# Performance work log

Hardware: AMD Instinct MI355X
Metric: run time of the kernel (lower is better)

The kernel has to match this reference:

```python
import jax, jax.numpy as jnp
import numpy as np

B, N, T, F, D, R, K, L, E = 4, 2000, 50, 10, 64, 8, 16, 3, 32


def setup_inputs() -> dict:
    key = jax.random.key(0)
    ks = jax.random.split(key, 12)
    rn = lambda k, shape, sc: (jax.random.normal(k, shape, jnp.float32) * sc)
    return {
        "X": jax.random.normal(ks[0], (B, N, T, F), jnp.float32),
        "neighbors": jax.random.randint(ks[1], (B, R, N, K), 0, N + 1),
        "gru_W": rn(ks[2], (F, 3 * D), 0.1),
        "gru_U": rn(ks[3], (D, 3 * D), 0.1),
        "gru_b": jnp.zeros((2, 3 * D), jnp.float32),
        "rel_emb": rn(ks[4], (R, E), 0.1),
        "proj_W": rn(ks[5], (R, D, D), 0.05),
        "proj_b": jnp.zeros((R, D), jnp.float32),
        "satt_W": rn(ks[6], (R, 2 * D + E), 0.05),
        "satt_b": jnp.zeros((R,), jnp.float32),
        "ratt_W": rn(ks[7], (2 * D + E,), 0.05),
        "ratt_b": jnp.zeros((), jnp.float32),
        "pred_W": rn(ks[8], (D, L), 0.05),
        "pred_b": jnp.zeros((L,), jnp.float32),
    }


def leaky(x):  # tf.nn.leaky_relu default alpha=0.2
    return jnp.where(x >= 0, x, 0.2 * x)


def gru(x, W, U, b):
    # Keras GRU (reset_after=True), gate order [z, r, h]. x: (M, T, F)
    xp = x @ W + b[0]                      # (M, T, 3D) input projections, precomputed
    h0 = jnp.zeros((x.shape[0], U.shape[0]), x.dtype)

    def step(h, xt):
        rec = h @ U + b[1]
        xz, xr, xh = jnp.split(xt, 3, axis=-1)
        rz, rr, rh = jnp.split(rec, 3, axis=-1)
        z = jax.nn.sigmoid(xz + rz)
        r = jax.nn.sigmoid(xr + rr)
        hh = jnp.tanh(xh + r * rh)
        return z * h + (1.0 - z) * hh, None

    h, _ = jax.lax.scan(step, h0, jnp.swapaxes(xp, 0, 1))
    return h


def reference(X, neighbors, gru_W, gru_U, gru_b, rel_emb, proj_W, proj_b,
              satt_W, satt_b, ratt_W, ratt_b, pred_W, pred_b):
    b, n, t, f = X.shape
    d = gru_U.shape[0]

    # --- GRU feature extraction (dropout inactive at inference) ---
    node = gru(X.reshape(b * n, t, f), gru_W, gru_U, gru_b).reshape(b, n, d)
    padded = jnp.concatenate([jnp.zeros((b, 1, d), node.dtype), node], axis=1)  # (B, N+1, D)

    # --- per-relation neighbor gather + projection ---
    neigh_raw = jax.vmap(lambda nf, idx: nf[idx])(padded, neighbors)            # (B, R, N, K, D)
    neigh = leaky(jnp.einsum('brnkd,rde->brnke', neigh_raw, proj_W)
                  + proj_b[None, :, None, None, :])                              # (B, R, N, K, D)

    cur = node                                                                   # (B, N, D)

    # --- state attention: Dense(1) on concat[cur, neigh, rel_emb], split weights ---
    w_cur, w_ngh, w_rel = satt_W[:, :d], satt_W[:, d:2 * d], satt_W[:, 2 * d:]
    s_cur = jnp.einsum('bnd,rd->brn', cur, w_cur)                                # (B, R, N)
    s_ngh = jnp.einsum('brnkd,rd->brnk', neigh, w_ngh)                           # (B, R, N, K)
    s_rel = jnp.einsum('re,re->r', rel_emb, w_rel) + satt_b                      # (R,)
    scores = leaky(s_cur[:, :, :, None] + s_ngh + s_rel[None, :, None, None])
    scores = scores + jnp.where(neighbors == 0, -1e9, 0.0).astype(scores.dtype)  # mask padding node
    att = jax.nn.softmax(scores, axis=-1)                                        # over K
    rel_rep = jnp.einsum('brnk,brnkd->brnd', att, neigh)                         # (B, R, N, D)

    # --- relation attention ---
    rep_t = jnp.transpose(rel_rep, (0, 2, 1, 3))                                 # (B, N, R, D)
    r_cur, r_rep, r_emb = ratt_W[:d], ratt_W[d:2 * d], ratt_W[2 * d:]
    rs = leaky(jnp.einsum('bnd,d->bn', cur, r_cur)[:, :, None]
               + jnp.einsum('bnrd,d->bnr', rep_t, r_rep)
               + (rel_emb @ r_emb)[None, None, :] + ratt_b)                      # (B, N, R)
    ratt = jax.nn.softmax(rs, axis=-1)
    agg = jnp.einsum('bnr,bnrd->bnd', ratt, rep_t)
    updated = cur + agg

    # --- prediction head ---
    return jax.nn.softmax(updated @ pred_W + pred_b)
```

## Files before the change

### kernel.cpp

```cpp
#include <hip/hip_runtime.h>
#include <hip/hip_bf16.h>
#include <cstddef>

constexpr int cB=4, cN=2000, cT=50, cF=10, cD=64, cR=8, cK=16, cE=32;
constexpr int NODES = cB*cN;
constexpr int N1    = cN+1;
constexpr int ROWS2 = cB*N1;

#define DEV static __device__ __forceinline__

typedef __attribute__((ext_vector_type(8))) short bf16x8;
typedef __attribute__((ext_vector_type(4))) float f32x4;
typedef __attribute__((ext_vector_type(4))) int   i32x4;

DEV float leaky(float x){ return fmaxf(x, 0.2f*x); }
DEV float wsumall(float v){
  v += __shfl_xor(v,32,64); v += __shfl_xor(v,16,64); v += __shfl_xor(v,8,64);
  v += __shfl_xor(v,4,64);  v += __shfl_xor(v,2,64);  v += __shfl_xor(v,1,64);
  return v;
}
DEV unsigned fu(float f){ return __float_as_uint(f); }
DEV float hif(float f){ return __uint_as_float(fu(f) & 0xFFFF0000u); }
DEV unsigned rne16(float f){
  unsigned u = fu(f);
  return (u + 0x7FFFu + ((u>>16)&1u)) >> 16;
}
DEV bf16x8 pack4(unsigned a, unsigned b, unsigned c2, unsigned d){
  union { i32x4 i; bf16x8 h; } u;
  u.i = (i32x4){(int)a,(int)b,(int)c2,(int)d};
  return u.h;
}
DEV unsigned PLO(unsigned x, unsigned y){ return __builtin_amdgcn_perm(y, x, 0x05040100u); }
DEV unsigned PHI(unsigned x, unsigned y){ return __builtin_amdgcn_perm(y, x, 0x07060302u); }
DEV f32x4 MF(bf16x8 a, bf16x8 b, f32x4 c){
  return __builtin_amdgcn_mfma_f32_16x16x32_bf16(a, b, c, 0, 0, 0);
}
DEV float bfu(unsigned short u){ return __uint_as_float(((unsigned)u)<<16); }

__global__ __launch_bounds__(256, 2) void k_gru(const float* __restrict__ X,
    const float* __restrict__ gW, const float* __restrict__ gU,
    const float* __restrict__ gb, const float* __restrict__ pW,
    const float* __restrict__ pb, const float* __restrict__ sattW,
    float* __restrict__ node, unsigned short* __restrict__ actb,
    float* __restrict__ sng2)
{
  __shared__ unsigned sH[2][1024];

  const int tid  = threadIdx.x;
  const int lane = tid & 63;
  const int w    = tid >> 6;
  const int c    = lane & 15;
  const int kg   = lane >> 4;
  const int nb   = (int)blockIdx.x * 16;
  const int col  = 16*w + c;
  const int bb   = nb / cN;

  bf16x8 BUhi[2][3], BUlo[2][3], BX[3];
  #pragma unroll
  for (int s=0;s<2;++s){
    #pragma unroll
    for (int cls=0; cls<3; ++cls){
      const int n = cls*64 + col;
      unsigned hi[4], lo[4];
      #pragma unroll
      for (int p=0;p<4;++p){
        float u0 = gU[(s*32 + kg*8 + 2*p    )*192 + n];
        float u1 = gU[(s*32 + kg*8 + 2*p + 1)*192 + n];
        hi[p] = (fu(u0)>>16) | (fu(u1) & 0xFFFF0000u);
        lo[p] = rne16(u0 - hif(u0)) | (rne16(u1 - hif(u1)) << 16);
      }
      BUhi[s][cls] = pack4(hi[0],hi[1],hi[2],hi[3]);
      BUlo[s][cls] = pack4(lo[0],lo[1],lo[2],lo[3]);
    }
  }
  #pragma unroll
  for (int cls=0; cls<3; ++cls){
    const int n = cls*64 + col;
    unsigned wd[4];
    #pragma unroll
    for (int p=0;p<4;++p){
      int f = kg*4 + p;
      unsigned v = (f < cF) ? rne16(gW[f*192 + n]) : 0u;
      wd[p] = v | (v << 16);
    }
    BX[cls] = pack4(wd[0],wd[1],wd[2],wd[3]);
  }

  const float bz  = gb[col]      + gb[192+col];
  const float br  = gb[64+col]   + gb[256+col];
  const float bh0 = gb[128+col];
  const float bh1 = gb[320+col];

  for (int i2 = tid; i2 < 1024; i2 += 256) sH[0][i2] = 0u;
  f32x4 ho = {0.f,0.f,0.f,0.f};
  __syncthreads();

  float xc[4], xn[4];
  const float* Xb = X + (size_t)(nb + c)*cT*cF;
  {
    #pragma unroll
    for (int p=0;p<4;++p){ int f = 4*kg+p; xc[p] = (f < cF) ? Xb[0*cF + f] : 0.f; }
    #pragma unroll
    for (int p=0;p<4;++p){ int f = 4*kg+p; xn[p] = (f < cF) ? Xb[1*cF + f] : 0.f; }
  }

  const unsigned sw  = (unsigned)((c&7)<<2);
  const unsigned rb0 = (unsigned)(c*64 + kg*8);

  for (int t = 0; t < cT; ++t){
    unsigned xw[4];
    #pragma unroll
    for (int p=0;p<4;++p)
      xw[p] = (fu(xc[p])>>16) | (rne16(xc[p] - hif(xc[p])) << 16);
    bf16x8 xf = pack4(xw[0],xw[1],xw[2],xw[3]);

    #pragma unroll
    for (int p=0;p<4;++p) xc[p] = xn[p];
    {
      int tn = (t+2 < cT) ? t+2 : cT-1;
      #pragma unroll
      for (int p=0;p<4;++p){ int f = 4*kg+p; xn[p] = (f < cF) ? Xb[(size_t)tn*cF + f] : 0.f; }
    }

    const unsigned* sr = sH[t & 1];
    i32x4 qa = *(const i32x4*)(sr + ((rb0 +  0) ^ sw));
    i32x4 qb = *(const i32x4*)(sr + ((rb0 +  4) ^ sw));
    i32x4 qc = *(const i32x4*)(sr + ((rb0 + 32) ^ sw));
    i32x4 qd = *(const i32x4*)(sr + ((rb0 + 36) ^ sw));
    bf16x8 hh0 = pack4(PLO(qa[0],qa[1]), PLO(qa[2],qa[3]), PLO(qb[0],qb[1]), PLO(qb[2],qb[3]));
    bf16x8 hl0 = pack4(PHI(qa[0],qa[1]), PHI(qa[2],qa[3]), PHI(qb[0],qb[1]), PHI(qb[2],qb[3]));
    bf16x8 hh1 = pack4(PLO(qc[0],qc[1]), PLO(qc[2],qc[3]), PLO(qd[0],qd[1]), PLO(qd[2],qd[3]));
    bf16x8 hl1 = pack4(PHI(qc[0],qc[1]), PHI(qc[2],qc[3]), PHI(qd[0],qd[1]), PHI(qd[2],qd[3]));

    f32x4 aZ  = {bz,bz,bz,bz};
    f32x4 aR  = {br,br,br,br};
    f32x4 aHc = {bh1,bh1,bh1,bh1};
    f32x4 aXh = {bh0,bh0,bh0,bh0};
    aZ  = MF(xf, BX[0], aZ);
    aR  = MF(xf, BX[1], aR);
    aXh = MF(xf, BX[2], aXh);
    aZ  = MF(hh0, BUhi[0][0], aZ);  aZ  = MF(hh1, BUhi[1][0], aZ);
    aR  = MF(hh0, BUhi[0][1], aR);  aR  = MF(hh1, BUhi[1][1], aR);
    aHc = MF(hh0, BUhi[0][2], aHc); aHc = MF(hh1, BUhi[1][2], aHc);
    aZ  = MF(hl0, BUhi[0][0], aZ);  aZ  = MF(hl1, BUhi[1][0], aZ);
    aR  = MF(hl0, BUhi[0][1], aR);  aR  = MF(hl1, BUhi[1][1], aR);
    aHc = MF(hl0, BUhi[0][2], aHc); aHc = MF(hl1, BUhi[1][2], aHc);
    aZ  = MF(hh0, BUlo[0][0], aZ);  aZ  = MF(hh1, BUlo[1][0], aZ);
    aR  = MF(hh0, BUlo[0][1], aR);  aR  = MF(hh1, BUlo[1][1], aR);
    aHc = MF(hh0, BUlo[0][2], aHc); aHc = MF(hh1, BUlo[1][2], aHc);

    unsigned* swr = sH[(t & 1) ^ 1];
    #pragma unroll
    for (int reg=0; reg<4; ++reg){
      float z  = __builtin_amdgcn_rcpf(1.0f + __expf(-aZ[reg]));
      float r  = __builtin_amdgcn_rcpf(1.0f + __expf(-aR[reg]));
      float pre = __builtin_fmaf(r, aHc[reg], aXh[reg]);
      float th = 1.0f - 2.0f*__builtin_amdgcn_rcpf(__expf(2.0f*pre) + 1.0f);
      float hn = __builtin_fmaf(z, ho[reg]-th, th);
      ho[reg] = hn;
      unsigned val = (fu(hn)>>16) | (rne16(hn - hif(hn)) << 16);
      int nodei = kg*4 + reg;
      swr[((unsigned)(nodei*64 + col)) ^ ((unsigned)((nodei&7)<<2))] = val;
    }
    asm volatile("s_waitcnt lgkmcnt(0)" ::: "memory");
    __builtin_amdgcn_s_barrier();
  }

  #pragma unroll
  for (int reg=0; reg<4; ++reg)
    node[(size_t)(nb + kg*4 + reg)*cD + col] = ho[reg];

  {
    const unsigned* sr = &sH[0][0];
    i32x4 qa = *(const i32x4*)(sr + ((rb0 +  0) ^ sw));
    i32x4 qb = *(const i32x4*)(sr + ((rb0 +  4) ^ sw));
    i32x4 qc = *(const i32x4*)(sr + ((rb0 + 32) ^ sw));
    i32x4 qd = *(const i32x4*)(sr + ((rb0 + 36) ^ sw));
    bf16x8 hh0 = pack4(PLO(qa[0],qa[1]), PLO(qa[2],qa[3]), PLO(qb[0],qb[1]), PLO(qb[2],qb[3]));
    bf16x8 hl0 = pack4(PHI(qa[0],qa[1]), PHI(qa[2],qa[3]), PHI(qb[0],qb[1]), PHI(qb[2],qb[3]));
    bf16x8 hh1 = pack4(PLO(qc[0],qc[1]), PLO(qc[2],qc[3]), PLO(qd[0],qd[1]), PLO(qd[2],qd[3]));
    bf16x8 hl1 = pack4(PHI(qc[0],qc[1]), PHI(qc[2],qc[3]), PHI(qd[0],qd[1]), PHI(qd[2],qd[3]));

    const int qbase = nb + bb + 1;
    #pragma unroll
    for (int r2=0; r2<2; ++r2){
      const int r = 2*w + r2;
      const float* Pr = pW + (size_t)r*cD*cD;
      bf16x8 PB[4][2];
      float pbv[4], wnv[4];
      #pragma unroll
      for (int cb=0; cb<4; ++cb){
        const int e = 16*cb + c;
        #pragma unroll
        for (int s=0;s<2;++s){
          unsigned wd[4];
          #pragma unroll
          for (int p=0;p<4;++p){
            int k0 = s*32 + kg*8 + 2*p;
            wd[p] = rne16(Pr[(size_t)k0*cD + e]) | (rne16(Pr[(size_t)(k0+1)*cD + e]) << 16);
          }
          PB[cb][s] = pack4(wd[0],wd[1],wd[2],wd[3]);
        }
        pbv[cb] = pb[r*cD + e];
        wnv[cb] = sattW[r*(2*cD+cE) + cD + e];
      }
      float sp[4] = {0.f,0.f,0.f,0.f};
      #pragma unroll
      for (int cb=0; cb<4; ++cb){
        f32x4 acc = {pbv[cb],pbv[cb],pbv[cb],pbv[cb]};
        acc = MF(hh0, PB[cb][0], acc); acc = MF(hh1, PB[cb][1], acc);
        acc = MF(hl0, PB[cb][0], acc); acc = MF(hl1, PB[cb][1], acc);
        #pragma unroll
        for (int reg=0; reg<4; ++reg){
          float o = leaky(acc[reg]);
          int qrow = qbase + kg*4 + reg;
          actb[((size_t)r*ROWS2 + qrow)*cD + 16*cb + c] = (unsigned short)rne16(o);
          sp[reg] = __builtin_fmaf(o, wnv[cb], sp[reg]);
        }
      }
      #pragma unroll
      for (int reg=0; reg<4; ++reg){
        float s2 = sp[reg];
        s2 += __shfl_xor(s2,1,64); s2 += __shfl_xor(s2,2,64);
        s2 += __shfl_xor(s2,4,64); s2 += __shfl_xor(s2,8,64);
        if (c == 0) sng2[(size_t)r*ROWS2 + qbase + kg*4 + reg] = s2;
      }
    }
  }

  if ((blockIdx.x % (cN/16)) == 0){
    #pragma unroll
    for (int r2=0; r2<2; ++r2){
      const int r = 2*w + r2;
      float v0 = leaky(pb[r*cD + lane]);
      float wv = sattW[r*(2*cD+cE) + cD + lane];
      actb[((size_t)r*ROWS2 + (size_t)bb*N1)*cD + lane] = (unsigned short)rne16(v0);
      float s2 = wsumall(v0 * wv);
      if (lane == 0) sng2[(size_t)r*ROWS2 + (size_t)bb*N1] = s2;
    }
  }
}

__global__ __launch_bounds__(256) void k_attn(const float* __restrict__ node,
    const int* __restrict__ nbrs, const float* __restrict__ sattW,
    const float* __restrict__ sattb, const float* __restrict__ rattW,
    const float* __restrict__ rattb, const float* __restrict__ predW,
    const float* __restrict__ predb, const float* __restrict__ relemb,
    const unsigned short* __restrict__ actb, const float* __restrict__ sng2,
    float* __restrict__ out)
{
  __shared__ float sSA[cR][cD];
  __shared__ float sSrel[cR], sRremb[cR];
  __shared__ float sAtt[4][cR][cK];
  __shared__ int   sOff[4][cR][cK];
  const int tid = threadIdx.x;
  for (int i=tid; i<cR*cD; i+=256) sSA[i>>6][i&63] = sattW[(i>>6)*(2*cD+cE) + (i&63)];
  if (tid < 64){
    int r = tid >> 3, j0 = (tid & 7)*4;
    float a = 0.f, b2 = 0.f;
    #pragma unroll
    for (int j=0;j<4;++j){
      float re = relemb[r*cE + j0 + j];
      a  += re * sattW[r*(2*cD+cE) + 2*cD + j0 + j];
      b2 += re * rattW[2*cD + j0 + j];
    }
    a  += __shfl_xor(a,1,64);  a  += __shfl_xor(a,2,64);  a  += __shfl_xor(a,4,64);
    b2 += __shfl_xor(b2,1,64); b2 += __shfl_xor(b2,2,64); b2 += __shfl_xor(b2,4,64);
    if ((tid & 7) == 0){ sSrel[r] = a + sattb[r]; sRremb[r] = b2; }
  }
  __syncthreads();

  const int wave = tid >> 6, lane = tid & 63;
  const int gn = (int)blockIdx.x*4 + wave;
  const int b = __builtin_amdgcn_readfirstlane(gn / cN);
  const int n = __builtin_amdgcn_readfirstlane(gn % cN);

  const float cur = node[(size_t)gn*cD + lane];

  float scr[8];
  #pragma unroll
  for (int r=0; r<8; ++r) scr[r] = wsumall(cur * sSA[r][lane]);

  const int g = lane >> 4, k = lane & 15;
  #pragma unroll
  for (int half=0; half<2; ++half){
    int r = half*4 + g;
    float sc0 = half==0 ? (g==0?scr[0]:g==1?scr[1]:g==2?scr[2]:scr[3])
                        : (g==0?scr[4]:g==1?scr[5]:g==2?scr[6]:scr[7]);
    int idx = nbrs[(((size_t)b*cR + r)*cN + n)*cK + k];
    int o = r*ROWS2 + b*N1 + idx;
    float sv = sng2[o];
    float sc = leaky(sc0 + sv + sSrel[r]);
// ... 30 lines not shown
  float rs[8];
  #pragma unroll
  for (int r=0; r<8; ++r) rs[r] = leaky(c0 + wsumall(facc[r]*rrep) + sRremb[r] + rb);
  float mx = rs[0];
  #pragma unroll
  for (int r=1; r<8; ++r) mx = fmaxf(mx, rs[r]);
  float es = 0.f; float ratt[8];
  #pragma unroll
  for (int r=0; r<8; ++r){ ratt[r] = __expf(rs[r]-mx); es += ratt[r]; }
  float inv = 1.f/es;
  float agg = 0.f;
  #pragma unroll
  for (int r=0; r<8; ++r) agg += (ratt[r]*inv) * facc[r];
  const float upd = cur + agg;

  float l0 = wsumall(upd * predW[lane*3 + 0]);
  float l1 = wsumall(upd * predW[lane*3 + 1]);
  float l2 = wsumall(upd * predW[lane*3 + 2]);
  if (lane == 0){
    l0 += predb[0]; l1 += predb[1]; l2 += predb[2];
    float m2 = fmaxf(l0, fmaxf(l1, l2));
    float e0 = __expf(l0-m2), e1 = __expf(l1-m2), e2 = __expf(l2-m2);
    float is = 1.f/(e0+e1+e2);
    out[(size_t)gn*3+0] = e0*is;
    out[(size_t)gn*3+1] = e1*is;
    out[(size_t)gn*3+2] = e2*is;
  }
}

extern "C" void kernel_launch(void* const* d_in, const int* in_sizes, int n_in,
                              void* d_out, int out_size, void* d_ws, size_t ws_size,
                              hipStream_t stream)
{
  const float* X      = (const float*)d_in[0];
  const int*   nbrs   = (const int*)  d_in[1];
  const float* gW     = (const float*)d_in[2];
  const float* gU     = (const float*)d_in[3];
  const float* gb     = (const float*)d_in[4];
  const float* relemb = (const float*)d_in[5];
  const float* pW     = (const float*)d_in[6];
  const float* pb     = (const float*)d_in[7];
  const float* sattW  = (const float*)d_in[8];
  const float* sattb  = (const float*)d_in[9];
  const float* rattW  = (const float*)d_in[10];
  const float* rattb  = (const float*)d_in[11];
  const float* predW  = (const float*)d_in[12];
  const float* predb  = (const float*)d_in[13];
  float* out = (float*)d_out;

  float*          node  = (float*)d_ws;
  unsigned short* actb  = (unsigned short*)(node + (size_t)NODES*cD);
  float*          sng2  = (float*)(actb + (size_t)cR*ROWS2*cD);

  k_gru <<<NODES/16, 256, 0, stream>>>(X, gW, gU, gb, pW, pb, sattW,
                                       node, actb, sng2);
  k_attn<<<NODES/4, 256, 0, stream>>>(node, nbrs, sattW, sattb, rattW, rattb,
                                      predW, predb, relemb, actb, sng2, out);
}
```

Baseline: 88.80 us.

## Split GRU recurrent K-dimension across two wave groups with LDS partial-sum exchange

```diff
diff --git a/kernel.cpp b/kernel.cpp
--- a/kernel.cpp
+++ b/kernel.cpp
@@ -32,12 +32,17 @@
 }
 DEV unsigned PLO(unsigned x, unsigned y){ return __builtin_amdgcn_perm(y, x, 0x05040100u); }
 DEV unsigned PHI(unsigned x, unsigned y){ return __builtin_amdgcn_perm(y, x, 0x07060302u); }
+DEV unsigned pack_hl3(float f){
+  float rem = f - hif(f);
+  return PHI(fu(f), fu(rem));
+}
 DEV f32x4 MF(bf16x8 a, bf16x8 b, f32x4 c){
   return __builtin_amdgcn_mfma_f32_16x16x32_bf16(a, b, c, 0, 0, 0);
 }
 DEV float bfu(unsigned short u){ return __uint_as_float(((unsigned)u)<<16); }
-
-__global__ __launch_bounds__(256, 2) void k_gru(const float* __restrict__ X,
+DEV float ex2(float x){ float r; asm("v_exp_f32 %0, %1" : "=v"(r) : "v"(x)); return r; }
+
+__global__ __launch_bounds__(512, 4) void k_gru(const float* __restrict__ X,
     const float* __restrict__ gW, const float* __restrict__ gU,
     const float* __restrict__ gb, const float* __restrict__ pW,
     const float* __restrict__ pb, const float* __restrict__ sattW,
@@ -45,53 +50,60 @@
     float* __restrict__ sng2)
 {
   __shared__ unsigned sH[2][1024];
+  __shared__ __align__(16) float pP[4][3][256];
 
   const int tid  = threadIdx.x;
   const int lane = tid & 63;
-  const int w    = tid >> 6;
+  const int w8   = tid >> 6;
+  const int w    = w8 & 3;
+  const bool owner = (w8 < 4);
+  const int s    = owner ? 0 : 1;
   const int c    = lane & 15;
   const int kg   = lane >> 4;
   const int nb   = (int)blockIdx.x * 16;
   const int col  = 16*w + c;
   const int bb   = nb / cN;
 
-  bf16x8 BUhi[2][3], BUlo[2][3], BX[3];
-  #pragma unroll
-  for (int s=0;s<2;++s){
-    #pragma unroll
-    for (int cls=0; cls<3; ++cls){
-      const int n = cls*64 + col;
-      unsigned hi[4], lo[4];
-      #pragma unroll
-      for (int p=0;p<4;++p){
-        float u0 = gU[(s*32 + kg*8 + 2*p    )*192 + n];
-        float u1 = gU[(s*32 + kg*8 + 2*p + 1)*192 + n];
-        hi[p] = (fu(u0)>>16) | (fu(u1) & 0xFFFF0000u);
-        lo[p] = rne16(u0 - hif(u0)) | (rne16(u1 - hif(u1)) << 16);
-      }
-      BUhi[s][cls] = pack4(hi[0],hi[1],hi[2],hi[3]);
-      BUlo[s][cls] = pack4(lo[0],lo[1],lo[2],lo[3]);
-    }
-  }
+  const float SZ = -1.4426950408889634f;
+  const float SH =  2.8853900817779268f;
+
+  const float scl0 = SZ, scl1 = SZ, scl2 = SH;
+  bf16x8 Uhi[3], Ulo[3], BXv[3];
   #pragma unroll
   for (int cls=0; cls<3; ++cls){
+    const float sc = (cls==2) ? scl2 : (cls==1 ? scl1 : scl0);
+    const int n = cls*64 + col;
+    unsigned hi[4], lo[4];
+    #pragma unroll
+    for (int p=0;p<4;++p){
+      float u0 = sc * gU[(s*32 + kg*8 + 2*p    )*192 + n];
+      float u1 = sc * gU[(s*32 + kg*8 + 2*p + 1)*192 + n];
+      hi[p] = (fu(u0)>>16) | (fu(u1) & 0xFFFF0000u);
+      lo[p] = rne16(u0 - hif(u0)) | (rne16(u1 - hif(u1)) << 16);
+    }
+    Uhi[cls] = pack4(hi[0],hi[1],hi[2],hi[3]);
+    Ulo[cls] = pack4(lo[0],lo[1],lo[2],lo[3]);
+  }
+  #pragma unroll
+  for (int cls=0; cls<3; ++cls){
+    const float sc = (cls==2) ? scl2 : scl0;
     const int n = cls*64 + col;
     unsigned wd[4];
     #pragma unroll
     for (int p=0;p<4;++p){
       int f = kg*4 + p;
-      unsigned v = (f < cF) ? rne16(gW[f*192 + n]) : 0u;
+      unsigned v = (f < cF) ? rne16(sc * gW[f*192 + n]) : 0u;
       wd[p] = v | (v << 16);
     }
-    BX[cls] = pack4(wd[0],wd[1],wd[2],wd[3]);
-  }
-
-  const float bz  = gb[col]      + gb[192+col];
-  const float br  = gb[64+col]   + gb[256+col];
-  const float bh0 = gb[128+col];
-  const float bh1 = gb[320+col];
-
-  for (int i2 = tid; i2 < 1024; i2 += 256) sH[0][i2] = 0u;
+    BXv[cls] = pack4(wd[0],wd[1],wd[2],wd[3]);
+  }
+
+  const float bz  = SZ*(gb[col]      + gb[192+col]);
+  const float br  = SZ*(gb[64+col]   + gb[256+col]);
+  const float bh0 = SH* gb[128+col];
+  const float bh1 = SH* gb[320+col];
+
+  for (int i2 = tid; i2 < 1024; i2 += 512) sH[0][i2] = 0u;
   f32x4 ho = {0.f,0.f,0.f,0.f};
   __syncthreads();
 
@@ -106,69 +118,94 @@
 
   const unsigned sw  = (unsigned)((c&7)<<2);
   const unsigned rb0 = (unsigned)(c*64 + kg*8);
+  float* pw0 = &pP[w][0][c*16 + kg*4];
+  float* pw1 = &pP[w][1][c*16 + kg*4];
+  float* pw2 = &pP[w][2][c*16 + kg*4];
 
   for (int t = 0; t < cT; ++t){
-    unsigned xw[4];
-    #pragma unroll
-    for (int p=0;p<4;++p)
-      xw[p] = (fu(xc[p])>>16) | (rne16(xc[p] - hif(xc[p])) << 16);
-    bf16x8 xf = pack4(xw[0],xw[1],xw[2],xw[3]);
-
-    #pragma unroll
-    for (int p=0;p<4;++p) xc[p] = xn[p];
-    {
-      int tn = (t+2 < cT) ? t+2 : cT-1;
+    const unsigned* sr = sH[t & 1];
+    f32x4 aZ, aR, aHc, aXh;
+    if (owner){
+      bf16x8 xf = pack4(pack_hl3(xc[0]), pack_hl3(xc[1]),
+                        pack_hl3(xc[2]), pack_hl3(xc[3]));
       #pragma unroll
-      for (int p=0;p<4;++p){ int f = 4*kg+p; xn[p] = (f < cF) ? Xb[(size_t)tn*cF + f] : 0.f; }
-    }
-
-    const unsigned* sr = sH[t & 1];
-    i32x4 qa = *(const i32x4*)(sr + ((rb0 +  0) ^ sw));
-    i32x4 qb = *(const i32x4*)(sr + ((rb0 +  4) ^ sw));
-    i32x4 qc = *(const i32x4*)(sr + ((rb0 + 32) ^ sw));
-    i32x4 qd = *(const i32x4*)(sr + ((rb0 + 36) ^ sw));
-    bf16x8 hh0 = pack4(PLO(qa[0],qa[1]), PLO(qa[2],qa[3]), PLO(qb[0],qb[1]), PLO(qb[2],qb[3]));
-    bf16x8 hl0 = pack4(PHI(qa[0],qa[1]), PHI(qa[2],qa[3]), PHI(qb[0],qb[1]), PHI(qb[2],qb[3]));
-    bf16x8 hh1 = pack4(PLO(qc[0],qc[1]), PLO(qc[2],qc[3]), PLO(qd[0],qd[1]), PLO(qd[2],qd[3]));
-    bf16x8 hl1 = pack4(PHI(qc[0],qc[1]), PHI(qc[2],qc[3]), PHI(qd[0],qd[1]), PHI(qd[2],qd[3]));
-
-    f32x4 aZ  = {bz,bz,bz,bz};
-    f32x4 aR  = {br,br,br,br};
-    f32x4 aHc = {bh1,bh1,bh1,bh1};
-    f32x4 aXh = {bh0,bh0,bh0,bh0};
-    aZ  = MF(xf, BX[0], aZ);
-    aR  = MF(xf, BX[1], aR);
-    aXh = MF(xf, BX[2], aXh);
-    aZ  = MF(hh0, BUhi[0][0], aZ);  aZ  = MF(hh1, BUhi[1][0], aZ);
-    aR  = MF(hh0, BUhi[0][1], aR);  aR  = MF(hh1, BUhi[1][1], aR);
-    aHc = MF(hh0, BUhi[0][2], aHc); aHc = MF(hh1, BUhi[1][2], aHc);
-    aZ  = MF(hl0, BUhi[0][0], aZ);  aZ  = MF(hl1, BUhi[1][0], aZ);
-    aR  = MF(hl0, BUhi[0][1], aR);  aR  = MF(hl1, BUhi[1][1], aR);
-    aHc = MF(hl0, BUhi[0][2], aHc); aHc = MF(hl1, BUhi[1][2], aHc);
-    aZ  = MF(hh0, BUlo[0][0], aZ);  aZ  = MF(hh1, BUlo[1][0], aZ);
-    aR  = MF(hh0, BUlo[0][1], aR);  aR  = MF(hh1, BUlo[1][1], aR);
-    aHc = MF(hh0, BUlo[0][2], aHc); aHc = MF(hh1, BUlo[1][2], aHc);
-
-    unsigned* swr = sH[(t & 1) ^ 1];
-    #pragma unroll
-    for (int reg=0; reg<4; ++reg){
-      float z  = __builtin_amdgcn_rcpf(1.0f + __expf(-aZ[reg]));
-      float r  = __builtin_amdgcn_rcpf(1.0f + __expf(-aR[reg]));
-      float pre = __builtin_fmaf(r, aHc[reg], aXh[reg]);
-      float th = 1.0f - 2.0f*__builtin_amdgcn_rcpf(__expf(2.0f*pre) + 1.0f);
-      float hn = __builtin_fmaf(z, ho[reg]-th, th);
-      ho[reg] = hn;
-      unsigned val = (fu(hn)>>16) | (rne16(hn - hif(hn)) << 16);
-      int nodei = kg*4 + reg;
-      swr[((unsigned)(nodei*64 + col)) ^ ((unsigned)((nodei&7)<<2))] = val;
+      for (int p=0;p<4;++p) xc[p] = xn[p];
+      {
+        int tn = (t+2 < cT) ? t+2 : cT-1;
+        #pragma unroll
+        for (int p=0;p<4;++p){ int f = 4*kg+p; xn[p] = (f < cF) ? Xb[(size_t)tn*cF + f] : 0.f; }
+      }
+      i32x4 qa = *(const i32x4*)(sr + ((rb0 +  0) ^ sw));
+      i32x4 qb = *(const i32x4*)(sr + ((rb0 +  4) ^ sw));
+      bf16x8 hh0 = pack4(PLO(qa[0],qa[1]), PLO(qa[2],qa[3]), PLO(qb[0],qb[1]), PLO(qb[2],qb[3]));
+      bf16x8 hl0 = pack4(PHI(qa[0],qa[1]), PHI(qa[2],qa[3]), PHI(qb[0],qb[1]), PHI(qb[2],qb[3]));
+      aZ  = (f32x4){bz,bz,bz,bz};
+      aR  = (f32x4){br,br,br,br};
+      aHc = (f32x4){bh1,bh1,bh1,bh1};
+      aXh = (f32x4){bh0,bh0,bh0,bh0};
+      aZ  = MF(xf, BXv[0], aZ);
+      aR  = MF(xf, BXv[1], aR);
+      aXh = MF(xf, BXv[2], aXh);
+      aZ  = MF(hh0, Uhi[0], aZ);
+      aR  = MF(hh0, Uhi[1], aR);
+      aHc = MF(hh0, Uhi[2], aHc);
+      aZ  = MF(hl0, Uhi[0], aZ);
+      aR  = MF(hl0, Uhi[1], aR);
+      aHc = MF(hl0, Uhi[2], aHc);
+      aZ  = MF(hh0, Ulo[0], aZ);
+      aR  = MF(hh0, Ulo[1], aR);
+      aHc = MF(hh0, Ulo[2], aHc);
+    } else {
+      i32x4 qc = *(const i32x4*)(sr + ((rb0 + 32) ^ sw));
+      i32x4 qd = *(const i32x4*)(sr + ((rb0 + 36) ^ sw));
+      bf16x8 hh1 = pack4(PLO(qc[0],qc[1]), PLO(qc[2],qc[3]), PLO(qd[0],qd[1]), PLO(qd[2],qd[3]));
+      bf16x8 hl1 = pack4(PHI(qc[0],qc[1]), PHI(qc[2],qc[3]), PHI(qd[0],qd[1]), PHI(qd[2],qd[3]));
+      f32x4 pz = {0.f,0.f,0.f,0.f}, pr = {0.f,0.f,0.f,0.f}, ph = {0.f,0.f,0.f,0.f};
+      pz = MF(hh1, Uhi[0], pz);
+      pr = MF(hh1, Uhi[1], pr);
+      ph = MF(hh1, Uhi[2], ph);
+      pz = MF(hl1, Uhi[0], pz);
+      pr = MF(hl1, Uhi[1], pr);
+      ph = MF(hl1, Uhi[2], ph);
+      pz = MF(hh1, Ulo[0], pz);
+      pr = MF(hh1, Ulo[1], pr);
+      ph = MF(hh1, Ulo[2], ph);
+      *(f32x4*)pw0 = pz;
+      *(f32x4*)pw1 = pr;
+      *(f32x4*)pw2 = ph;
     }
     asm volatile("s_waitcnt lgkmcnt(0)" ::: "memory");
     __builtin_amdgcn_s_barrier();
-  }
-
-  #pragma unroll
-  for (int reg=0; reg<4; ++reg)
-    node[(size_t)(nb + kg*4 + reg)*cD + col] = ho[reg];
+
+    if (owner){
+      f32x4 p0 = *(const f32x4*)pw0;
+      f32x4 p1 = *(const f32x4*)pw1;
+      f32x4 p2 = *(const f32x4*)pw2;
+      aZ  = aZ  + p0;
+      aR  = aR  + p1;
+      aHc = aHc + p2;
+      unsigned* swr = sH[(t & 1) ^ 1];
+      #pragma unroll
+      for (int reg=0; reg<4; ++reg){
+        float z   = __builtin_amdgcn_rcpf(1.0f + ex2(aZ[reg]));
+        float r   = __builtin_amdgcn_rcpf(1.0f + ex2(aR[reg]));
+        float phv = __builtin_fmaf(r, aHc[reg], aXh[reg]);
+        float th  = __builtin_fmaf(-2.0f, __builtin_amdgcn_rcpf(ex2(phv) + 1.0f), 1.0f);
+        float hn  = __builtin_fmaf(z, ho[reg]-th, th);
+        ho[reg] = hn;
+        int nodei = kg*4 + reg;
+        swr[((unsigned)(nodei*64 + col)) ^ ((unsigned)((nodei&7)<<2))] = pack_hl3(hn);
+      }
+    }
+    asm volatile("s_waitcnt lgkmcnt(0)" ::: "memory");
+    __builtin_amdgcn_s_barrier();
+  }
+
+  if (owner){
+    #pragma unroll
+    for (int reg=0; reg<4; ++reg)
+      node[(size_t)(nb + kg*4 + reg)*cD + col] = ho[reg];
+  }
 
   {
     const unsigned* sr = &sH[0][0];
@@ -182,62 +219,56 @@
     bf16x8 hl1 = pack4(PHI(qc[0],qc[1]), PHI(qc[2],qc[3]), PHI(qd[0],qd[1]), PHI(qd[2],qd[3]));
 
     const int qbase = nb + bb + 1;
-    #pragma unroll
-    for (int r2=0; r2<2; ++r2){
-      const int r = 2*w + r2;
-      const float* Pr = pW + (size_t)r*cD*cD;
-      bf16x8 PB[4][2];
-      float pbv[4], wnv[4];
+    const int r = w8;
+    const float* Pr = pW + (size_t)r*cD*cD;
+    bf16x8 PB[4][2];
+    float pbv[4], wnv[4];
+    #pragma unroll
+    for (int cb=0; cb<4; ++cb){
+      const int e = 16*cb + c;
       #pragma unroll
-      for (int cb=0; cb<4; ++cb){
-        const int e = 16*cb + c;
+      for (int s2=0;s2<2;++s2){
+        unsigned wd[4];
         #pragma unroll
-        for (int s=0;s<2;++s){
-          unsigned wd[4];
-          #pragma unroll
-          for (int p=0;p<4;++p){
-            int k0 = s*32 + kg*8 + 2*p;
-            wd[p] = rne16(Pr[(size_t)k0*cD + e]) | (rne16(Pr[(size_t)(k0+1)*cD + e]) << 16);
-          }
-          PB[cb][s] = pack4(wd[0],wd[1],wd[2],wd[3]);
+        for (int p=0;p<4;++p){
+          int k0 = s2*32 + kg*8 + 2*p;
+          wd[p] = rne16(Pr[(size_t)k0*cD + e]) | (rne16(Pr[(size_t)(k0+1)*cD + e]) << 16);
         }
-        pbv[cb] = pb[r*cD + e];
-        wnv[cb] = sattW[r*(2*cD+cE) + cD + e];
+        PB[cb][s2] = pack4(wd[0],wd[1],wd[2],wd[3]);
       }
-      float sp[4] = {0.f,0.f,0.f,0.f};
-      #pragma unroll
-      for (int cb=0; cb<4; ++cb){
-        f32x4 acc = {pbv[cb],pbv[cb],pbv[cb],pbv[cb]};
-        acc = MF(hh0, PB[cb][0], acc); acc = MF(hh1, PB[cb][1], acc);
-        acc = MF(hl0, PB[cb][0], acc); acc = MF(hl1, PB[cb][1], acc);
-        #pragma unroll
-        for (int reg=0; reg<4; ++reg){
-          float o = leaky(acc[reg]);
-          int qrow = qbase + kg*4 + reg;
-          actb[((size_t)r*ROWS2 + qrow)*cD + 16*cb + c] = (unsigned short)rne16(o);
-          sp[reg] = __builtin_fmaf(o, wnv[cb], sp[reg]);
-        }
-      }
+      pbv[cb] = pb[r*cD + e];
+      wnv[cb] = sattW[r*(2*cD+cE) + cD + e];
+    }
+    float sp[4] = {0.f,0.f,0.f,0.f};
+    #pragma unroll
+    for (int cb=0; cb<4; ++cb){
+      f32x4 acc = {pbv[cb],pbv[cb],pbv[cb],pbv[cb]};
+      acc = MF(hh0, PB[cb][0], acc); acc = MF(hh1, PB[cb][1], acc);
+      acc = MF(hl0, PB[cb][0], acc); acc = MF(hl1, PB[cb][1], acc);
       #pragma unroll
       for (int reg=0; reg<4; ++reg){
-        float s2 = sp[reg];
-        s2 += __shfl_xor(s2,1,64); s2 += __shfl_xor(s2,2,64);
-        s2 += __shfl_xor(s2,4,64); s2 += __shfl_xor(s2,8,64);
-        if (c == 0) sng2[(size_t)r*ROWS2 + qbase + kg*4 + reg] = s2;
+        float o = leaky(acc[reg]);
+        int qrow = qbase + kg*4 + reg;
+        actb[((size_t)r*ROWS2 + qrow)*cD + 16*cb + c] = (unsigned short)rne16(o);
+        sp[reg] = __builtin_fmaf(o, wnv[cb], sp[reg]);
       }
     }
+    #pragma unroll
+    for (int reg=0; reg<4; ++reg){
+      float s2 = sp[reg];
+      s2 += __shfl_xor(s2,1,64); s2 += __shfl_xor(s2,2,64);
+      s2 += __shfl_xor(s2,4,64); s2 += __shfl_xor(s2,8,64);
+      if (c == 0) sng2[(size_t)r*ROWS2 + qbase + kg*4 + reg] = s2;
+    }
   }
 
   if ((blockIdx.x % (cN/16)) == 0){
-    #pragma unroll
-    for (int r2=0; r2<2; ++r2){
-      const int r = 2*w + r2;
-      float v0 = leaky(pb[r*cD + lane]);
-      float wv = sattW[r*(2*cD+cE) + cD + lane];
-      actb[((size_t)r*ROWS2 + (size_t)bb*N1)*cD + lane] = (unsigned short)rne16(v0);
-      float s2 = wsumall(v0 * wv);
-      if (lane == 0) sng2[(size_t)r*ROWS2 + (size_t)bb*N1] = s2;
-    }
+    const int r = w8;
+    float v0 = leaky(pb[r*cD + lane]);
+    float wv = sattW[r*(2*cD+cE) + cD + lane];
+    actb[((size_t)r*ROWS2 + (size_t)bb*N1)*cD + lane] = (unsigned short)rne16(v0);
+    float s2 = wsumall(v0 * wv);
+    if (lane == 0) sng2[(size_t)r*ROWS2 + (size_t)bb*N1] = s2;
   }
 }
 
@@ -374,7 +405,7 @@
   unsigned short* actb  = (unsigned short*)(node + (size_t)NODES*cD);
   float*          sng2  = (float*)(actb + (size_t)cR*ROWS2*cD);
 
-  k_gru <<<NODES/16, 256, 0, stream>>>(X, gW, gU, gb, pW, pb, sattW,
+  k_gru <<<NODES/16, 512, 0, stream>>>(X, gW, gU, gb, pW, pb, sattW,
                                        node, actb, sng2);
   k_attn<<<NODES/4, 256, 0, stream>>>(node, nbrs, sattW, sattb, rattW, rattb,
                                       predW, predb, relemb, actb, sng2, out);
```

After: 94.13 us. 6.0% more time.

## Process two independent node tiles per GRU block and fold exp scaling into weights

Applied to the files above, without the earlier changes.

```diff
diff --git a/kernel.cpp b/kernel.cpp
--- a/kernel.cpp
+++ b/kernel.cpp
@@ -32,40 +32,52 @@
 }
 DEV unsigned PLO(unsigned x, unsigned y){ return __builtin_amdgcn_perm(y, x, 0x05040100u); }
 DEV unsigned PHI(unsigned x, unsigned y){ return __builtin_amdgcn_perm(y, x, 0x07060302u); }
+DEV unsigned pack_hl3(float f){
+  float rem = f - hif(f);
+  return PHI(fu(f), fu(rem));
+}
 DEV f32x4 MF(bf16x8 a, bf16x8 b, f32x4 c){
   return __builtin_amdgcn_mfma_f32_16x16x32_bf16(a, b, c, 0, 0, 0);
 }
 DEV float bfu(unsigned short u){ return __uint_as_float(((unsigned)u)<<16); }
-
-__global__ __launch_bounds__(256, 2) void k_gru(const float* __restrict__ X,
+DEV float ex2(float x){ float r; asm("v_exp_f32 %0, %1" : "=v"(r) : "v"(x)); return r; }
+
+__global__ __launch_bounds__(256, 1) void k_gru(const float* __restrict__ X,
     const float* __restrict__ gW, const float* __restrict__ gU,
     const float* __restrict__ gb, const float* __restrict__ pW,
     const float* __restrict__ pb, const float* __restrict__ sattW,
     float* __restrict__ node, unsigned short* __restrict__ actb,
     float* __restrict__ sng2)
 {
-  __shared__ unsigned sH[2][1024];
+  __shared__ unsigned sHA[2][1024];
+  __shared__ unsigned sHB[2][1024];
 
   const int tid  = threadIdx.x;
   const int lane = tid & 63;
   const int w    = tid >> 6;
   const int c    = lane & 15;
   const int kg   = lane >> 4;
-  const int nb   = (int)blockIdx.x * 16;
+  const int nbA  = (int)blockIdx.x * 32;
+  const int nbB  = nbA + 16;
   const int col  = 16*w + c;
-  const int bb   = nb / cN;
+  const int bbA  = nbA / cN;
+  const int bbB  = nbB / cN;
+
+  const float SZ = -1.4426950408889634f;
+  const float SH =  2.8853900817779268f;
 
   bf16x8 BUhi[2][3], BUlo[2][3], BX[3];
   #pragma unroll
   for (int s=0;s<2;++s){
     #pragma unroll
     for (int cls=0; cls<3; ++cls){
+      const float sc = (cls==2) ? SH : SZ;
       const int n = cls*64 + col;
       unsigned hi[4], lo[4];
       #pragma unroll
       for (int p=0;p<4;++p){
-        float u0 = gU[(s*32 + kg*8 + 2*p    )*192 + n];
-        float u1 = gU[(s*32 + kg*8 + 2*p + 1)*192 + n];
+        float u0 = sc * gU[(s*32 + kg*8 + 2*p    )*192 + n];
+        float u1 = sc * gU[(s*32 + kg*8 + 2*p + 1)*192 + n];
         hi[p] = (fu(u0)>>16) | (fu(u1) & 0xFFFF0000u);
         lo[p] = rne16(u0 - hif(u0)) | (rne16(u1 - hif(u1)) << 16);
       }
@@ -75,116 +87,176 @@
   }
   #pragma unroll
   for (int cls=0; cls<3; ++cls){
+    const float sc = (cls==2) ? SH : SZ;
     const int n = cls*64 + col;
     unsigned wd[4];
     #pragma unroll
     for (int p=0;p<4;++p){
       int f = kg*4 + p;
-      unsigned v = (f < cF) ? rne16(gW[f*192 + n]) : 0u;
+      unsigned v = (f < cF) ? rne16(sc * gW[f*192 + n]) : 0u;
       wd[p] = v | (v << 16);
     }
     BX[cls] = pack4(wd[0],wd[1],wd[2],wd[3]);
   }
 
-  const float bz  = gb[col]      + gb[192+col];
-  const float br  = gb[64+col]   + gb[256+col];
-  const float bh0 = gb[128+col];
-  const float bh1 = gb[320+col];
-
-  for (int i2 = tid; i2 < 1024; i2 += 256) sH[0][i2] = 0u;
-  f32x4 ho = {0.f,0.f,0.f,0.f};
+  const float bz  = SZ*(gb[col]      + gb[192+col]);
+  const float br  = SZ*(gb[64+col]   + gb[256+col]);
+  const float bh0 = SH* gb[128+col];
+  const float bh1 = SH* gb[320+col];
+
+  for (int i2 = tid; i2 < 1024; i2 += 256){ sHA[0][i2] = 0u; sHB[0][i2] = 0u; }
+  f32x4 hoA = {0.f,0.f,0.f,0.f}, hoB = {0.f,0.f,0.f,0.f};
   __syncthreads();
 
-  float xc[4], xn[4];
-  const float* Xb = X + (size_t)(nb + c)*cT*cF;
+  float xcA[4], xnA[4], xcB[4], xnB[4];
+  const float* XbA = X + (size_t)(nbA + c)*cT*cF;
+  const float* XbB = X + (size_t)(nbB + c)*cT*cF;
   {
     #pragma unroll
-    for (int p=0;p<4;++p){ int f = 4*kg+p; xc[p] = (f < cF) ? Xb[0*cF + f] : 0.f; }
-    #pragma unroll
-    for (int p=0;p<4;++p){ int f = 4*kg+p; xn[p] = (f < cF) ? Xb[1*cF + f] : 0.f; }
+    for (int p=0;p<4;++p){ int f = 4*kg+p;
+      xcA[p] = (f < cF) ? XbA[0*cF + f] : 0.f;
+      xnA[p] = (f < cF) ? XbA[1*cF + f] : 0.f;
+      xcB[p] = (f < cF) ? XbB[0*cF + f] : 0.f;
+      xnB[p] = (f < cF) ? XbB[1*cF + f] : 0.f;
+    }
   }
 
   const unsigned sw  = (unsigned)((c&7)<<2);
   const unsigned rb0 = (unsigned)(c*64 + kg*8);
 
   for (int t = 0; t < cT; ++t){
-    unsigned xw[4];
-    #pragma unroll
-    for (int p=0;p<4;++p)
-      xw[p] = (fu(xc[p])>>16) | (rne16(xc[p] - hif(xc[p])) << 16);
-    bf16x8 xf = pack4(xw[0],xw[1],xw[2],xw[3]);
-
-    #pragma unroll
-    for (int p=0;p<4;++p) xc[p] = xn[p];
+    const int tn = (t+2 < cT) ? t+2 : cT-1;
     {
-      int tn = (t+2 < cT) ? t+2 : cT-1;
-      #pragma unroll
-      for (int p=0;p<4;++p){ int f = 4*kg+p; xn[p] = (f < cF) ? Xb[(size_t)tn*cF + f] : 0.f; }
-    }
-
-    const unsigned* sr = sH[t & 1];
-    i32x4 qa = *(const i32x4*)(sr + ((rb0 +  0) ^ sw));
-    i32x4 qb = *(const i32x4*)(sr + ((rb0 +  4) ^ sw));
-    i32x4 qc = *(const i32x4*)(sr + ((rb0 + 32) ^ sw));
-    i32x4 qd = *(const i32x4*)(sr + ((rb0 + 36) ^ sw));
-    bf16x8 hh0 = pack4(PLO(qa[0],qa[1]), PLO(qa[2],qa[3]), PLO(qb[0],qb[1]), PLO(qb[2],qb[3]));
-    bf16x8 hl0 = pack4(PHI(qa[0],qa[1]), PHI(qa[2],qa[3]), PHI(qb[0],qb[1]), PHI(qb[2],qb[3]));
-    bf16x8 hh1 = pack4(PLO(qc[0],qc[1]), PLO(qc[2],qc[3]), PLO(qd[0],qd[1]), PLO(qd[2],qd[3]));
-    bf16x8 hl1 = pack4(PHI(qc[0],qc[1]), PHI(qc[2],qc[3]), PHI(qd[0],qd[1]), PHI(qd[2],qd[3]));
-
-    f32x4 aZ  = {bz,bz,bz,bz};
-    f32x4 aR  = {br,br,br,br};
-    f32x4 aHc = {bh1,bh1,bh1,bh1};
-    f32x4 aXh = {bh0,bh0,bh0,bh0};
-    aZ  = MF(xf, BX[0], aZ);
-    aR  = MF(xf, BX[1], aR);
-    aXh = MF(xf, BX[2], aXh);
-    aZ  = MF(hh0, BUhi[0][0], aZ);  aZ  = MF(hh1, BUhi[1][0], aZ);
-    aR  = MF(hh0, BUhi[0][1], aR);  aR  = MF(hh1, BUhi[1][1], aR);
-    aHc = MF(hh0, BUhi[0][2], aHc); aHc = MF(hh1, BUhi[1][2], aHc);
-    aZ  = MF(hl0, BUhi[0][0], aZ);  aZ  = MF(hl1, BUhi[1][0], aZ);
-    aR  = MF(hl0, BUhi[0][1], aR);  aR  = MF(hl1, BUhi[1][1], aR);
-    aHc = MF(hl0, BUhi[0][2], aHc); aHc = MF(hl1, BUhi[1][2], aHc);
-    aZ  = MF(hh0, BUlo[0][0], aZ);  aZ  = MF(hh1, BUlo[1][0], aZ);
-    aR  = MF(hh0, BUlo[0][1], aR);  aR  = MF(hh1, BUlo[1][1], aR);
-    aHc = MF(hh0, BUlo[0][2], aHc); aHc = MF(hh1, BUlo[1][2], aHc);
-
-    unsigned* swr = sH[(t & 1) ^ 1];
-    #pragma unroll
-    for (int reg=0; reg<4; ++reg){
-      float z  = __builtin_amdgcn_rcpf(1.0f + __expf(-aZ[reg]));
-      float r  = __builtin_amdgcn_rcpf(1.0f + __expf(-aR[reg]));
-      float pre = __builtin_fmaf(r, aHc[reg], aXh[reg]);
-      float th = 1.0f - 2.0f*__builtin_amdgcn_rcpf(__expf(2.0f*pre) + 1.0f);
-      float hn = __builtin_fmaf(z, ho[reg]-th, th);
-      ho[reg] = hn;
-      unsigned val = (fu(hn)>>16) | (rne16(hn - hif(hn)) << 16);
-      int nodei = kg*4 + reg;
-      swr[((unsigned)(nodei*64 + col)) ^ ((unsigned)((nodei&7)<<2))] = val;
+      bf16x8 xf = pack4(pack_hl3(xcA[0]), pack_hl3(xcA[1]),
+                        pack_hl3(xcA[2]), pack_hl3(xcA[3]));
+      #pragma unroll
+      for (int p=0;p<4;++p) xcA[p] = xnA[p];
+      #pragma unroll
+      for (int p=0;p<4;++p){ int f = 4*kg+p; xnA[p] = (f < cF) ? XbA[(size_t)tn*cF + f] : 0.f; }
+
+      const unsigned* sr = sHA[t & 1];
+      i32x4 qa = *(const i32x4*)(sr + ((rb0 +  0) ^ sw));
+      i32x4 qb = *(const i32x4*)(sr + ((rb0 +  4) ^ sw));
+      i32x4 qc = *(const i32x4*)(sr + ((rb0 + 32) ^ sw));
+      i32x4 qd = *(const i32x4*)(sr + ((rb0 + 36) ^ sw));
+      bf16x8 hh0 = pack4(PLO(qa[0],qa[1]), PLO(qa[2],qa[3]), PLO(qb[0],qb[1]), PLO(qb[2],qb[3]));
+      bf16x8 hl0 = pack4(PHI(qa[0],qa[1]), PHI(qa[2],qa[3]), PHI(qb[0],qb[1]), PHI(qb[2],qb[3]));
+      bf16x8 hh1 = pack4(PLO(qc[0],qc[1]), PLO(qc[2],qc[3]), PLO(qd[0],qd[1]), PLO(qd[2],qd[3]));
+      bf16x8 hl1 = pack4(PHI(qc[0],qc[1]), PHI(qc[2],qc[3]), PHI(qd[0],qd[1]), PHI(qd[2],qd[3]));
+
+      f32x4 aZ  = {bz,bz,bz,bz};
+      f32x4 aR  = {br,br,br,br};
+      f32x4 aHc = {bh1,bh1,bh1,bh1};
+      f32x4 aXh = {bh0,bh0,bh0,bh0};
+      aZ  = MF(xf, BX[0], aZ);
+      aR  = MF(xf, BX[1], aR);
+      aXh = MF(xf, BX[2], aXh);
+      aZ  = MF(hh0, BUhi[0][0], aZ);  aZ  = MF(hh1, BUhi[1][0], aZ);
+      aR  = MF(hh0, BUhi[0][1], aR);  aR  = MF(hh1, BUhi[1][1], aR);
+      aHc = MF(hh0, BUhi[0][2], aHc); aHc = MF(hh1, BUhi[1][2], aHc);
+      aZ  = MF(hl0, BUhi[0][0], aZ);  aZ  = MF(hl1, BUhi[1][0], aZ);
+      aR  = MF(hl0, BUhi[0][1], aR);  aR  = MF(hl1, BUhi[1][1], aR);
+      aHc = MF(hl0, BUhi[0][2], aHc); aHc = MF(hl1, BUhi[1][2], aHc);
+      aZ  = MF(hh0, BUlo[0][0], aZ);  aZ  = MF(hh1, BUlo[1][0], aZ);
+      aR  = MF(hh0, BUlo[0][1], aR);  aR  = MF(hh1, BUlo[1][1], aR);
+      aHc = MF(hh0, BUlo[0][2], aHc); aHc = MF(hh1, BUlo[1][2], aHc);
+
+      unsigned* swr = sHA[(t & 1) ^ 1];
+      #pragma unroll
+      for (int reg=0; reg<4; ++reg){
+        float z   = __builtin_amdgcn_rcpf(1.0f + ex2(aZ[reg]));
+        float r   = __builtin_amdgcn_rcpf(1.0f + ex2(aR[reg]));
+        float phv = __builtin_fmaf(r, aHc[reg], aXh[reg]);
+        float th  = __builtin_fmaf(-2.0f, __builtin_amdgcn_rcpf(ex2(phv) + 1.0f), 1.0f);
+        float hn  = __builtin_fmaf(z, hoA[reg]-th, th);
+        hoA[reg] = hn;
+        int nodei = kg*4 + reg;
+        swr[((unsigned)(nodei*64 + col)) ^ ((unsigned)((nodei&7)<<2))] = pack_hl3(hn);
+      }
+    }
+    {
+      bf16x8 xf = pack4(pack_hl3(xcB[0]), pack_hl3(xcB[1]),
+                        pack_hl3(xcB[2]), pack_hl3(xcB[3]));
+      #pragma unroll
+      for (int p=0;p<4;++p) xcB[p] = xnB[p];
+      #pragma unroll
+      for (int p=0;p<4;++p){ int f = 4*kg+p; xnB[p] = (f < cF) ? XbB[(size_t)tn*cF + f] : 0.f; }
+
+      const unsigned* sr = sHB[t & 1];
+      i32x4 qa = *(const i32x4*)(sr + ((rb0 +  0) ^ sw));
+      i32x4 qb = *(const i32x4*)(sr + ((rb0 +  4) ^ sw));
+      i32x4 qc = *(const i32x4*)(sr + ((rb0 + 32) ^ sw));
+      i32x4 qd = *(const i32x4*)(sr + ((rb0 + 36) ^ sw));
+      bf16x8 hh0 = pack4(PLO(qa[0],qa[1]), PLO(qa[2],qa[3]), PLO(qb[0],qb[1]), PLO(qb[2],qb[3]));
+      bf16x8 hl0 = pack4(PHI(qa[0],qa[1]), PHI(qa[2],qa[3]), PHI(qb[0],qb[1]), PHI(qb[2],qb[3]));
+      bf16x8 hh1 = pack4(PLO(qc[0],qc[1]), PLO(qc[2],qc[3]), PLO(qd[0],qd[1]), PLO(qd[2],qd[3]));
+      bf16x8 hl1 = pack4(PHI(qc[0],qc[1]), PHI(qc[2],qc[3]), PHI(qd[0],qd[1]), PHI(qd[2],qd[3]));
+
+      f32x4 aZ  = {bz,bz,bz,bz};
+      f32x4 aR  = {br,br,br,br};
+      f32x4 aHc = {bh1,bh1,bh1,bh1};
+      f32x4 aXh = {bh0,bh0,bh0,bh0};
+      aZ  = MF(xf, BX[0], aZ);
+      aR  = MF(xf, BX[1], aR);
+      aXh = MF(xf, BX[2], aXh);
+      aZ  = MF(hh0, BUhi[0][0], aZ);  aZ  = MF(hh1, BUhi[1][0], aZ);
+      aR  = MF(hh0, BUhi[0][1], aR);  aR  = MF(hh1, BUhi[1][1], aR);
+      aHc = MF(hh0, BUhi[0][2], aHc); aHc = MF(hh1, BUhi[1][2], aHc);
+      aZ  = MF(hl0, BUhi[0][0], aZ);  aZ  = MF(hl1, BUhi[1][0], aZ);
+      aR  = MF(hl0, BUhi[0][1], aR);  aR  = MF(hl1, BUhi[1][1], aR);
+      aHc = MF(hl0, BUhi[0][2], aHc); aHc = MF(hl1, BUhi[1][2], aHc);
+      aZ  = MF(hh0, BUlo[0][0], aZ);  aZ  = MF(hh1, BUlo[1][0], aZ);
+      aR  = MF(hh0, BUlo[0][1], aR);  aR  = MF(hh1, BUlo[1][1], aR);
+      aHc = MF(hh0, BUlo[0][2], aHc); aHc = MF(hh1, BUlo[1][2], aHc);
+
+      unsigned* swr = sHB[(t & 1) ^ 1];
+      #pragma unroll
+      for (int reg=0; reg<4; ++reg){
+        float z   = __builtin_amdgcn_rcpf(1.0f + ex2(aZ[reg]));
+        float r   = __builtin_amdgcn_rcpf(1.0f + ex2(aR[reg]));
+        float phv = __builtin_fmaf(r, aHc[reg], aXh[reg]);
+        float th  = __builtin_fmaf(-2.0f, __builtin_amdgcn_rcpf(ex2(phv) + 1.0f), 1.0f);
+        float hn  = __builtin_fmaf(z, hoB[reg]-th, th);
+        hoB[reg] = hn;
+        int nodei = kg*4 + reg;
+        swr[((unsigned)(nodei*64 + col)) ^ ((unsigned)((nodei&7)<<2))] = pack_hl3(hn);
+      }
     }
     asm volatile("s_waitcnt lgkmcnt(0)" ::: "memory");
     __builtin_amdgcn_s_barrier();
   }
 
   #pragma unroll
-  for (int reg=0; reg<4; ++reg)
-    node[(size_t)(nb + kg*4 + reg)*cD + col] = ho[reg];
+  for (int reg=0; reg<4; ++reg){
+    node[(size_t)(nbA + kg*4 + reg)*cD + col] = hoA[reg];
+    node[(size_t)(nbB + kg*4 + reg)*cD + col] = hoB[reg];
+  }
 
   {
-    const unsigned* sr = &sH[0][0];
-    i32x4 qa = *(const i32x4*)(sr + ((rb0 +  0) ^ sw));
-    i32x4 qb = *(const i32x4*)(sr + ((rb0 +  4) ^ sw));
-    i32x4 qc = *(const i32x4*)(sr + ((rb0 + 32) ^ sw));
-    i32x4 qd = *(const i32x4*)(sr + ((rb0 + 36) ^ sw));
-    bf16x8 hh0 = pack4(PLO(qa[0],qa[1]), PLO(qa[2],qa[3]), PLO(qb[0],qb[1]), PLO(qb[2],qb[3]));
-    bf16x8 hl0 = pack4(PHI(qa[0],qa[1]), PHI(qa[2],qa[3]), PHI(qb[0],qb[1]), PHI(qb[2],qb[3]));
-    bf16x8 hh1 = pack4(PLO(qc[0],qc[1]), PLO(qc[2],qc[3]), PLO(qd[0],qd[1]), PLO(qd[2],qd[3]));
-    bf16x8 hl1 = pack4(PHI(qc[0],qc[1]), PHI(qc[2],qc[3]), PHI(qd[0],qd[1]), PHI(qd[2],qd[3]));
-
-    const int qbase = nb + bb + 1;
-    #pragma unroll
-    for (int r2=0; r2<2; ++r2){
-      const int r = 2*w + r2;
+    const unsigned* srA = &sHA[0][0];
+    i32x4 qa = *(const i32x4*)(srA + ((rb0 +  0) ^ sw));
+    i32x4 qb = *(const i32x4*)(srA + ((rb0 +  4) ^ sw));
+    i32x4 qc = *(const i32x4*)(srA + ((rb0 + 32) ^ sw));
+    i32x4 qd = *(const i32x4*)(srA + ((rb0 + 36) ^ sw));
+    bf16x8 hh0A = pack4(PLO(qa[0],qa[1]), PLO(qa[2],qa[3]), PLO(qb[0],qb[1]), PLO(qb[2],qb[3]));
+    bf16x8 hl0A = pack4(PHI(qa[0],qa[1]), PHI(qa[2],qa[3]), PHI(qb[0],qb[1]), PHI(qb[2],qb[3]));
+    bf16x8 hh1A = pack4(PLO(qc[0],qc[1]), PLO(qc[2],qc[3]), PLO(qd[0],qd[1]), PLO(qd[2],qd[3]));
+    bf16x8 hl1A = pack4(PHI(qc[0],qc[1]), PHI(qc[2],qc[3]), PHI(qd[0],qd[1]), PHI(qd[2],qd[3]));
+    const unsigned* srB = &sHB[0][0];
+    qa = *(const i32x4*)(srB + ((rb0 +  0) ^ sw));
+    qb = *(const i32x4*)(srB + ((rb0 +  4) ^ sw));
+    qc = *(const i32x4*)(srB + ((rb0 + 32) ^ sw));
+    qd = *(const i32x4*)(srB + ((rb0 + 36) ^ sw));
+    bf16x8 hh0B = pack4(PLO(qa[0],qa[1]), PLO(qa[2],qa[3]), PLO(qb[0],qb[1]), PLO(qb[2],qb[3]));
+    bf16x8 hl0B = pack4(PHI(qa[0],qa[1]), PHI(qa[2],qa[3]), PHI(qb[0],qb[1]), PHI(qb[2],qb[3]));
+    bf16x8 hh1B = pack4(PLO(qc[0],qc[1]), PLO(qc[2],qc[3]), PLO(qd[0],qd[1]), PLO(qd[2],qd[3]));
+    bf16x8 hl1B = pack4(PHI(qc[0],qc[1]), PHI(qc[2],qc[3]), PHI(qd[0],qd[1]), PHI(qd[2],qd[3]));
+
+    const int qbaseA = nbA + bbA + 1;
+    const int qbaseB = nbB + bbB + 1;
+    #pragma unroll
+    for (int rr=0; rr<2; ++rr){
+      const int r = 2*w + rr;
       const float* Pr = pW + (size_t)r*cD*cD;
       bf16x8 PB[4][2];
       float pbv[4], wnv[4];
@@ -192,51 +264,87 @@
       for (int cb=0; cb<4; ++cb){
         const int e = 16*cb + c;
         #pragma unroll
-        for (int s=0;s<2;++s){
+        for (int s2=0;s2<2;++s2){
           unsigned wd[4];
           #pragma unroll
           for (int p=0;p<4;++p){
-            int k0 = s*32 + kg*8 + 2*p;
+            int k0 = s2*32 + kg*8 + 2*p;
             wd[p] = rne16(Pr[(size_t)k0*cD + e]) | (rne16(Pr[(size_t)(k0+1)*cD + e]) << 16);
           }
-          PB[cb][s] = pack4(wd[0],wd[1],wd[2],wd[3]);
+          PB[cb][s2] = pack4(wd[0],wd[1],wd[2],wd[3]);
         }
         pbv[cb] = pb[r*cD + e];
         wnv[cb] = sattW[r*(2*cD+cE) + cD + e];
       }
-      float sp[4] = {0.f,0.f,0.f,0.f};
-      #pragma unroll
-      for (int cb=0; cb<4; ++cb){
-        f32x4 acc = {pbv[cb],pbv[cb],pbv[cb],pbv[cb]};
-        acc = MF(hh0, PB[cb][0], acc); acc = MF(hh1, PB[cb][1], acc);
-        acc = MF(hl0, PB[cb][0], acc); acc = MF(hl1, PB[cb][1], acc);
+      {
+        float sp[4] = {0.f,0.f,0.f,0.f};
+        #pragma unroll
+        for (int cb=0; cb<4; ++cb){
+          f32x4 acc = {pbv[cb],pbv[cb],pbv[cb],pbv[cb]};
+          acc = MF(hh0A, PB[cb][0], acc); acc = MF(hh1A, PB[cb][1], acc);
+          acc = MF(hl0A, PB[cb][0], acc); acc = MF(hl1A, PB[cb][1], acc);
+          #pragma unroll
+          for (int reg=0; reg<4; ++reg){
+            float o = leaky(acc[reg]);
+            int qrow = qbaseA + kg*4 + reg;
+            actb[((size_t)r*ROWS2 + qrow)*cD + 16*cb + c] = (unsigned short)rne16(o);
+            sp[reg] = __builtin_fmaf(o, wnv[cb], sp[reg]);
+          }
+        }
         #pragma unroll
         for (int reg=0; reg<4; ++reg){
-          float o = leaky(acc[reg]);
-          int qrow = qbase + kg*4 + reg;
-          actb[((size_t)r*ROWS2 + qrow)*cD + 16*cb + c] = (unsigned short)rne16(o);
-          sp[reg] = __builtin_fmaf(o, wnv[cb], sp[reg]);
+          float s2 = sp[reg];
+          s2 += __shfl_xor(s2,1,64); s2 += __shfl_xor(s2,2,64);
+          s2 += __shfl_xor(s2,4,64); s2 += __shfl_xor(s2,8,64);
+          if (c == 0) sng2[(size_t)r*ROWS2 + qbaseA + kg*4 + reg] = s2;
         }
       }
-      #pragma unroll
-      for (int reg=0; reg<4; ++reg){
-        float s2 = sp[reg];
-        s2 += __shfl_xor(s2,1,64); s2 += __shfl_xor(s2,2,64);
-        s2 += __shfl_xor(s2,4,64); s2 += __shfl_xor(s2,8,64);
-        if (c == 0) sng2[(size_t)r*ROWS2 + qbase + kg*4 + reg] = s2;
-      }
-    }
-  }
-
-  if ((blockIdx.x % (cN/16)) == 0){
-    #pragma unroll
-    for (int r2=0; r2<2; ++r2){
-      const int r = 2*w + r2;
+      {
+        float sp[4] = {0.f,0.f,0.f,0.f};
+        #pragma unroll
+        for (int cb=0; cb<4; ++cb){
+          f32x4 acc = {pbv[cb],pbv[cb],pbv[cb],pbv[cb]};
+          acc = MF(hh0B, PB[cb][0], acc); acc = MF(hh1B, PB[cb][1], acc);
+          acc = MF(hl0B, PB[cb][0], acc); acc = MF(hl1B, PB[cb][1], acc);
+          #pragma unroll
+          for (int reg=0; reg<4; ++reg){
+            float o = leaky(acc[reg]);
+            int qrow = qbaseB + kg*4 + reg;
+            actb[((size_t)r*ROWS2 + qrow)*cD + 16*cb + c] = (unsigned short)rne16(o);
+            sp[reg] = __builtin_fmaf(o, wnv[cb], sp[reg]);
+          }
+        }
+        #pragma unroll
+        for (int reg=0; reg<4; ++reg){
+          float s2 = sp[reg];
+          s2 += __shfl_xor(s2,1,64); s2 += __shfl_xor(s2,2,64);
+          s2 += __shfl_xor(s2,4,64); s2 += __shfl_xor(s2,8,64);
+          if (c == 0) sng2[(size_t)r*ROWS2 + qbaseB + kg*4 + reg] = s2;
+        }
+      }
+    }
+  }
+
+  if ((nbA % cN) == 0){
+    #pragma unroll
+    for (int rr=0; rr<2; ++rr){
+      const int r = 2*w + rr;
       float v0 = leaky(pb[r*cD + lane]);
       float wv = sattW[r*(2*cD+cE) + cD + lane];
-      actb[((size_t)r*ROWS2 + (size_t)bb*N1)*cD + lane] = (unsigned short)rne16(v0);
+      actb[((size_t)r*ROWS2 + (size_t)bbA*N1)*cD + lane] = (unsigned short)rne16(v0);
       float s2 = wsumall(v0 * wv);
-      if (lane == 0) sng2[(size_t)r*ROWS2 + (size_t)bb*N1] = s2;
+      if (lane == 0) sng2[(size_t)r*ROWS2 + (size_t)bbA*N1] = s2;
+    }
+  }
+  if ((nbB % cN) == 0){
+    #pragma unroll
+    for (int rr=0; rr<2; ++rr){
+      const int r = 2*w + rr;
+      float v0 = leaky(pb[r*cD + lane]);
+      float wv = sattW[r*(2*cD+cE) + cD + lane];
+      actb[((size_t)r*ROWS2 + (size_t)bbB*N1)*cD + lane] = (unsigned short)rne16(v0);
+      float s2 = wsumall(v0 * wv);
+      if (lane == 0) sng2[(size_t)r*ROWS2 + (size_t)bbB*N1] = s2;
     }
   }
 }
@@ -374,7 +482,7 @@
   unsigned short* actb  = (unsigned short*)(node + (size_t)NODES*cD);
   float*          sng2  = (float*)(actb + (size_t)cR*ROWS2*cD);
 
-  k_gru <<<NODES/16, 256, 0, stream>>>(X, gW, gU, gb, pW, pb, sattW,
+  k_gru <<<NODES/32, 256, 0, stream>>>(X, gW, gU, gb, pW, pb, sattW,
                                        node, actb, sng2);
   k_attn<<<NODES/4, 256, 0, stream>>>(node, nbrs, sattW, sattb, rattW, rattb,
                                       predW, predb, relemb, actb, sng2, out);
```

New measurement: 99.91 us. 12.5% more time.
